# Optimization experiments

Measured on AMD Instinct MI355X. Metric: run time of the kernel, lower is better.

## Reference

```python
import jax, jax.numpy as jnp
import numpy as np

B, S, D = 2, 2048, 2048
G, HPG = 4, 4            # n_groups, heads_per_group (n_heads=16)
DH = D // (G * HPG)      # head dim d_q = d_k = d_v = 128


def setup_inputs() -> dict:
    key = jax.random.key(0)
    ks = jax.random.split(key, 14)
    s = 1.0 / np.sqrt(D)
    inp = {
        "query": jax.random.normal(ks[0], (B, S, D), jnp.float32),
        "key":   jax.random.normal(ks[1], (B, S, D), jnp.float32),
        "value": jax.random.normal(ks[2], (B, S, D), jnp.float32),
        # per-group, per-head Q projections; per-group shared K, V
        "WQ": jax.random.normal(ks[3], (G, HPG, DH, D), jnp.float32) * s,
        "bQ": jax.random.normal(ks[4], (G, HPG, DH), jnp.float32) * 0.01,
        "WK": jax.random.normal(ks[5], (G, DH, D), jnp.float32) * s,
        "bK": jax.random.normal(ks[6], (G, DH), jnp.float32) * 0.01,
        "WV": jax.random.normal(ks[7], (G, DH, D), jnp.float32) * s,
        "bV": jax.random.normal(ks[8], (G, DH), jnp.float32) * 0.01,
        "WO": jax.random.normal(ks[9], (D, G * HPG * DH), jnp.float32) * s,
        "bO": jax.random.normal(ks[10], (D,), jnp.float32) * 0.01,
    }
    return inp


def reference(query, key, value, WQ, bQ, WK, bK, WV, bV, WO, bO):
    # q: [B, G, HPG, S, DH] — all per-head Q projections as one batched GEMM
    q = jnp.einsum('bsd,ghqd->bghsq', query, WQ) + bQ[None, :, :, None, :]
    # k, v: [B, G, S, DH] — one K/V per group (shared across heads in group)
    k = jnp.einsum('bsd,gkd->bgsk', key, WK) + bK[None, :, None, :]
    v = jnp.einsum('bsd,gvd->bgsv', value, WV) + bV[None, :, None, :]
    scale = 1.0 / jnp.sqrt(jnp.asarray(DH, q.dtype))
    # scores: [B, G, HPG, S_q, S_k]
    scores = jnp.einsum('bghsq,bgtq->bghst', q, k) * scale
    attn = jax.nn.softmax(scores, axis=-1)
    out = jnp.einsum('bghst,bgtv->bghsv', attn, v)   # [B, G, HPG, S, DH]
    # concat heads group-major, then transpose(1,2) + flatten like the torch code
    out = out.reshape(B, G * HPG, S, DH).transpose(0, 2, 1, 3).reshape(B, S, G * HPG * DH)
    return out @ WO.T + bO
```

## Files before the change

kernel.cpp:

```cpp
#include <hip/hip_runtime.h>
#include <cstdint>
#include <cstddef>


typedef __attribute__((ext_vector_type(8)))  __bf16 bf16x8;
typedef __attribute__((ext_vector_type(4)))  __bf16 bf16x4;
typedef __attribute__((ext_vector_type(4)))  float  f32x4;
typedef __attribute__((ext_vector_type(16))) float  f32x16;
typedef __attribute__((ext_vector_type(4)))  unsigned int u32x4;

#define GLD16(gp, lp) __builtin_amdgcn_global_load_lds(                         \
    (__attribute__((address_space(1))) void*)(size_t)(gp),                     \
    (__attribute__((address_space(3))) void*)(lp), 16, 0, 0)

#define PLSWAP(a, b) asm volatile("v_permlane32_swap_b32 %0, %1" : "+v"(a), "+v"(b))
#define EXP2F(x) __builtin_amdgcn_exp2f(x)

static __device__ __forceinline__ unsigned pack2bf(float a, float b) {
    unsigned short ua = __builtin_bit_cast(unsigned short, (__bf16)a);
    unsigned short ub = __builtin_bit_cast(unsigned short, (__bf16)b);
    return (unsigned)ua | ((unsigned)ub << 16);
}

__global__ void f2b_kernel(const float* __restrict__ in, __bf16* __restrict__ out, long n8) {
    long stride = (long)gridDim.x * blockDim.x;
    for (long i = (long)blockIdx.x * blockDim.x + threadIdx.x; i < n8; i += stride) {
        const float4* p = (const float4*)(in + i * 8);
        float4 a = p[0], b = p[1];
        bf16x8 r;
        r[0] = (__bf16)a.x; r[1] = (__bf16)a.y; r[2] = (__bf16)a.z; r[3] = (__bf16)a.w;
        r[4] = (__bf16)b.x; r[5] = (__bf16)b.y; r[6] = (__bf16)b.z; r[7] = (__bf16)b.w;
        *(bf16x8*)(out + i * 8) = r;
    }
}

template <int OUTF32>
__global__ __launch_bounds__(512)
void gemm256(const __bf16* __restrict__ A, const __bf16* __restrict__ Bm,
             const float* __restrict__ bias, float* __restrict__ Cf,
             __bf16* __restrict__ Cb, int M, int N, int K, int nbx) {
    __shared__ __bf16 As[3][256 * 64];
    __shared__ __bf16 Bs[3][128 * 64];
    const int tid = threadIdx.x, lane = tid & 63, wid = tid >> 6;
    const int g = lane >> 4, c = lane & 15;
    const int wr = wid >> 1, wc = wid & 1;
    const int cpx = gridDim.x >> 3;
    const int swz = ((int)blockIdx.x & 7) * cpx + ((int)blockIdx.x >> 3);
    const int bx = swz % nbx, by = swz / nbx;
    const int m0 = by * 256, n0 = bx * 128;
    const int nkt = K >> 6;

    const f32x4 z = {0.f, 0.f, 0.f, 0.f};
    f32x4 acc[4][4];
#pragma unroll
    for (int i = 0; i < 4; ++i)
#pragma unroll
        for (int j = 0; j < 4; ++j) acc[i][j] = z;

    auto stageA = [&](int b, int kt, int h) {
        if (kt >= nkt) return;
        const __bf16* src = A + (size_t)m0 * K + (size_t)kt * 64;
#pragma unroll
        for (int i = 0; i < 2; ++i) {
            int ci = h * 1024 + i * 512 + tid;
            int row = ci >> 3, chg = (ci & 7) ^ (row & 7);
            GLD16(src + (size_t)row * K + chg * 8, &As[b][ci * 8]);
        }
    };
    auto stageB = [&](int b, int kt) {
        if (kt >= nkt) return;
        const __bf16* src = Bm + (size_t)n0 * K + (size_t)kt * 64;
#pragma unroll
        for (int i = 0; i < 2; ++i) {
            int ci = i * 512 + tid;
            int row = ci >> 3, chg = (ci & 7) ^ (row & 7);
            GLD16(src + (size_t)row * K + chg * 8, &Bs[b][ci * 8]);
        }
    };

    stageA(0, 0, 0); stageA(0, 0, 1); stageB(0, 0);
    stageA(1, 1, 0); stageA(1, 1, 1); stageB(1, 1);
    asm volatile("s_waitcnt vmcnt(6)" ::: "memory");
    __builtin_amdgcn_sched_barrier(0);
    __builtin_amdgcn_s_barrier();

    int bd = 0;
    for (int kt = 0; kt < nkt; ++kt) {
        const int bs = (bd >= 1) ? bd - 1 : 2;
        bf16x8 af[4], bfr[4];
#pragma unroll
        for (int ph = 0; ph < 2; ++ph) {
#pragma unroll
            for (int mi = 0; mi < 4; ++mi) {
                int row = wr * 64 + mi * 16 + c;
                int ch = (ph * 4 + g) ^ (c & 7);
                af[mi] = *(const bf16x8*)&As[bd][row * 64 + ch * 8];
            }
#pragma unroll
            for (int ni = 0; ni < 4; ++ni) {
                int row = wc * 64 + ni * 16 + c;
                int ch = (ph * 4 + g) ^ (c & 7);
                bfr[ni] = *(const bf16x8*)&Bs[bd][row * 64 + ch * 8];
            }
            if (ph == 0) {
                stageA(bs, kt + 2, 0);
            } else {
                stageA(bs, kt + 2, 1);
                stageB(bs, kt + 2);
            }
            __builtin_amdgcn_s_barrier();
            asm volatile("s_waitcnt lgkmcnt(0)" ::: "memory");
            __builtin_amdgcn_sched_barrier(0);
            __builtin_amdgcn_s_setprio(1);
#pragma unroll
            for (int mi = 0; mi < 4; ++mi)
#pragma unroll
                for (int ni = 0; ni < 4; ++ni)
                    acc[mi][ni] = __builtin_amdgcn_mfma_f32_16x16x32_bf16(
                        af[mi], bfr[ni], acc[mi][ni], 0, 0, 0);
            __builtin_amdgcn_s_setprio(0);
            if (ph == 1) {
                if (kt >= nkt - 2) asm volatile("s_waitcnt vmcnt(0)" ::: "memory");
                else               asm volatile("s_waitcnt vmcnt(6)" ::: "memory");
                __builtin_amdgcn_sched_barrier(0);
            }
            __builtin_amdgcn_s_barrier();
        }
        bd = (bd >= 2) ? 0 : bd + 1;
    }

#pragma unroll
    for (int mi = 0; mi < 4; ++mi) {
#pragma unroll
        for (int ni = 0; ni < 4; ++ni) {
            int col = n0 + wc * 64 + ni * 16 + c;
            float bvc = bias[col];
#pragma unroll
            for (int r = 0; r < 4; ++r) {
                int row = m0 + wr * 64 + mi * 16 + g * 4 + r;
                float v = acc[mi][ni][r] + bvc;
                if (OUTF32) Cf[(size_t)row * N + col] = v;
                else        Cb[(size_t)row * N + col] = (__bf16)v;
            }
        }
    }
}

static __device__ __forceinline__
void gemm_tile(const __bf16* __restrict__ A, const __bf16* __restrict__ Bm,
               const float* __restrict__ bias,
               __bf16* __restrict__ Cb, int N, int K, int m0, int n0, int biasrow,
               __bf16* As, __bf16* Bs) {
    const int tid = threadIdx.x;
    const int lane = tid & 63, wid = tid >> 6;
    const int g = lane >> 4, c = lane & 15;
    const int wr = wid >> 1, wc = wid & 1;

    const f32x4 z = {0.f, 0.f, 0.f, 0.f};
    f32x4 acc[4][4];
#pragma unroll
    for (int i = 0; i < 4; ++i)
#pragma unroll
        for (int j = 0; j < 4; ++j) acc[i][j] = z;

    const int nk = K >> 5;
#pragma unroll
    for (int i = 0; i < 2; ++i) {
        int ci = i * 256 + tid, row = ci >> 2, kc = (ci & 3) * 8;
        GLD16(A + (size_t)(m0 + row) * K + kc, As + ci * 8);
        GLD16(Bm + (size_t)(n0 + row) * K + kc, Bs + ci * 8);
    }
    __syncthreads();

    int cur = 0;
    for (int t = 0; t < nk; ++t) {
        if (t + 1 < nk) {
            int koff = (t + 1) * 32;
            int nb = (cur ^ 1) * 4096;
#pragma unroll
            for (int i = 0; i < 2; ++i) {
                int ci = i * 256 + tid, row = ci >> 2, kc = (ci & 3) * 8;
                GLD16(A + (size_t)(m0 + row) * K + koff + kc, As + nb + ci * 8);
                GLD16(Bm + (size_t)(n0 + row) * K + koff + kc, Bs + nb + ci * 8);
            }
        }
        int cb = cur * 4096;
        bf16x8 af[4], bfv[4];
#pragma unroll
        for (int im = 0; im < 4; ++im)
            af[im] = *(const bf16x8*)&As[cb + (wr * 64 + im * 16 + c) * 32 + g * 8];
#pragma unroll
        for (int in = 0; in < 4; ++in)
            bfv[in] = *(const bf16x8*)&Bs[cb + (wc * 64 + in * 16 + c) * 32 + g * 8];
        __builtin_amdgcn_s_setprio(1);
#pragma unroll
        for (int im = 0; im < 4; ++im)
#pragma unroll
            for (int in = 0; in < 4; ++in)
                acc[im][in] = __builtin_amdgcn_mfma_f32_16x16x32_bf16(
                    af[im], bfv[in], acc[im][in], 0, 0, 0);
        __builtin_amdgcn_s_setprio(0);
        __syncthreads();
        cur ^= 1;
    }

#pragma unroll
    for (int im = 0; im < 4; ++im) {
#pragma unroll
        for (int in = 0; in < 4; ++in) {
            int col = n0 + wc * 64 + in * 16 + c;
            float bvc = biasrow ? 0.f : bias[col];
#pragma unroll
            for (int r = 0; r < 4; ++r) {
                int row = m0 + wr * 64 + im * 16 + g * 4 + r;
                float v = acc[im][in][r] + (biasrow ? bias[row] : bvc);
                Cb[(size_t)row * N + col] = (__bf16)v;
            }
        }
    }
}

__global__ __launch_bounds__(256)
void gemm_kv(const __bf16* __restrict__ kb, const __bf16* __restrict__ wkb,
             const float* __restrict__ bK, __bf16* __restrict__ kp,
             const __bf16* __restrict__ wvb, const __bf16* __restrict__ vb,
             const float* __restrict__ bV, __bf16* __restrict__ vpT) {
    __shared__ __bf16 As[2 * 128 * 32];
    __shared__ __bf16 Bs[2 * 128 * 32];
    const int bid = blockIdx.x;
    const int swz = (bid & 7) * 32 + (bid >> 3);
    if (swz < 128) {
        int bx = swz & 31, by = swz >> 5;
        gemm_tile(kb, wkb, bK, kp, 512, 2048, bx * 128, by * 128, 0, As, Bs);
    } else {
        int s2 = swz - 128;
        int bx = s2 & 3, by = s2 >> 2;
        gemm_tile(wvb, vb, bV, vpT, 4096, 2048, bx * 128, by * 128, 1, As, Bs);
    }
}

__global__ __launch_bounds__(256)
void attn_kernel(const __bf16* __restrict__ Qw, const __bf16* __restrict__ Kw,
                 const __bf16* __restrict__ VTw, __bf16* __restrict__ Ow) {
    constexpr int S = 2048, DQ = 2048, DKV = 512, TOK = 4096;
    const int bid = blockIdx.x;
    const int xcd = bid & 7, slot = bid >> 3;
    const int b = xcd >> 2, grp = xcd & 3;
    const int head = grp * 4 + (slot & 3);
    const int qblk = slot >> 2;
    const __bf16* Q   = Qw + (size_t)b * S * DQ + head * 128;
    const __bf16* Kp  = Kw + (size_t)b * S * DKV + grp * 128;
    const __bf16* VTp = VTw + (size_t)(grp * 128) * TOK + (size_t)b * S;
    __bf16* Op = Ow + (size_t)b * S * DQ + head * 128;

    __shared__ __bf16 Ks[2][64 * 128];
    __shared__ __bf16 Vs[2][128 * 64];

    const int tid = threadIdx.x, wid = tid >> 6, lane = tid & 63;
    const int ql = lane & 31, hi = lane >> 5;
    const int qrow = qblk * 128 + wid * 32 + ql;

    bf16x8 qf[8];
#pragma unroll
    for (int ks = 0; ks < 8; ++ks)
        qf[ks] = *(const bf16x8*)(Q + (size_t)qrow * DQ + ks * 16 + hi * 8);

    f32x16 o[4];
#pragma unroll
    for (int d = 0; d < 4; ++d)
#pragma unroll
        for (int r = 0; r < 16; ++r) o[d][r] = 0.f;
    float mprev = -1e30f, lsum = 0.f;
    constexpr float kexp = 0.08838834764831845f * 1.4426950408889634f;
    constexpr float THR = 8.0f / kexp;

    auto stage = [&](int buf, int t) {
#pragma unroll
        for (int i = 0; i < 4; ++i) {
            int ci = i * 256 + tid;
            int key = ci >> 4, ccl = ci & 15, ccg = ccl ^ (key & 15);
            GLD16(Kp + (size_t)(t * 64 + key) * DKV + ccg * 8, &Ks[buf][ci * 8]);
        }
#pragma unroll
        for (int i = 0; i < 4; ++i) {
            int ci = i * 256 + tid;
            int dh = ci >> 3, cl = ci & 7, cg = cl ^ ((dh ^ (dh >> 3)) & 7);
            GLD16(VTp + (size_t)dh * TOK + t * 64 + cg * 8, &Vs[buf][ci * 8]);
        }
    };

    stage(0, 0);
    __syncthreads();

    const int nt = S / 64;
    int cur = 0;
    for (int t = 0; t < nt; ++t) {
        if (t + 1 < nt) stage(cur ^ 1, t + 1);

        f32x16 sc[2];
        __builtin_amdgcn_s_setprio(1);
#pragma unroll
        for (int kt = 0; kt < 2; ++kt) {
#pragma unroll
            for (int r = 0; r < 16; ++r) sc[kt][r] = 0.f;
#pragma unroll
            for (int ks = 0; ks < 8; ++ks) {
                int key = kt * 32 + ql;
                int chl = (ks * 2 + hi) ^ (key & 15);
                bf16x8 kf = *(const bf16x8*)&Ks[cur][key * 128 + chl * 8];
                sc[kt] = __builtin_amdgcn_mfma_f32_32x32x16_bf16(kf, qf[ks], sc[kt], 0, 0, 0);
            }
        }
        __builtin_amdgcn_s_setprio(0);

        float mo = sc[0][0];
#pragma unroll
        for (int r = 1; r < 16; ++r) mo = fmaxf(mo, sc[0][r]);
#pragma unroll
        for (int r = 0; r < 16; ++r) mo = fmaxf(mo, sc[1][r]);
        mo = fmaxf(mo, __shfl_xor(mo, 32, 64));
        if (!__all(mo - mprev <= THR)) {
            float mn = fmaxf(mprev, mo);
            float ef = EXP2F((mprev - mn) * kexp);
            lsum *= ef;
#pragma unroll
            for (int d = 0; d < 4; ++d)
#pragma unroll
                for (int r = 0; r < 16; ++r) o[d][r] *= ef;
            mprev = mn;
        }
        float mnk = mprev * kexp;
        float rs = 0.f;
#pragma unroll
        for (int kt = 0; kt < 2; ++kt)
#pragma unroll
            for (int r = 0; r < 16; ++r) {
                float p = EXP2F(__builtin_fmaf(sc[kt][r], kexp, -mnk));
                sc[kt][r] = p;
                rs += p;
            }
        rs += __shfl_xor(rs, 32, 64);
        lsum += rs;

        unsigned pk[2][4][2];
#pragma unroll
        for (int kt = 0; kt < 2; ++kt)
#pragma unroll
            for (int rg = 0; rg < 4; ++rg) {
                pk[kt][rg][0] = pack2bf(sc[kt][rg * 4 + 0], sc[kt][rg * 4 + 1]);
                pk[kt][rg][1] = pack2bf(sc[kt][rg * 4 + 2], sc[kt][rg * 4 + 3]);
            }

        __builtin_amdgcn_s_setprio(1);
#pragma unroll
        for (int ks = 0; ks < 4; ++ks) {
            const int kt = ks >> 1, e = ks & 1;
            unsigned a0 = pk[kt][2 * e][0], b0 = pk[kt][2 * e + 1][0];
            unsigned a1 = pk[kt][2 * e][1], b1 = pk[kt][2 * e + 1][1];
            PLSWAP(a0, b0);
            PLSWAP(a1, b1);
            u32x4 fw = {a0, a1, b0, b1};
            bf16x8 pf = __builtin_bit_cast(bf16x8, fw);
#pragma unroll
            for (int dht = 0; dht < 4; ++dht) {
                int dh = dht * 32 + ql;
                int chl = (ks * 2 + hi) ^ ((dh ^ (dh >> 3)) & 7);
                bf16x8 vf = *(const bf16x8*)&Vs[cur][dh * 64 + chl * 8];
                o[dht] = __builtin_amdgcn_mfma_f32_32x32x16_bf16(vf, pf, o[dht], 0, 0, 0);
            }
        }
        __builtin_amdgcn_s_setprio(0);
        __syncthreads();
        cur ^= 1;
    }

    float inv = 1.0f / lsum;
#pragma unroll
    for (int dht = 0; dht < 4; ++dht)
#pragma unroll
        for (int rg = 0; rg < 4; ++rg) {
            bf16x4 wv;
#pragma unroll
            for (int j = 0; j < 4; ++j) wv[j] = (__bf16)(o[dht][rg * 4 + j] * inv);
            int dh0 = dht * 32 + rg * 8 + hi * 4;
            *(bf16x4*)(Op + (size_t)qrow * DQ + dh0) = wv;
        }
}

extern "C" void kernel_launch(void* const* d_in, const int* in_sizes, int n_in,
                              void* d_out, int out_size, void* d_ws, size_t ws_size,
                              hipStream_t stream) {
    (void)in_sizes; (void)n_in; (void)out_size; (void)ws_size;
    const float* query = (const float*)d_in[0];
    const float* key   = (const float*)d_in[1];
    const float* value = (const float*)d_in[2];
    const float* WQ = (const float*)d_in[3];
    const float* bQ = (const float*)d_in[4];
    const float* WK = (const float*)d_in[5];
    const float* bK = (const float*)d_in[6];
    const float* WV = (const float*)d_in[7];
    const float* bV = (const float*)d_in[8];
    const float* WO = (const float*)d_in[9];
    const float* bO = (const float*)d_in[10];
    float* out = (float*)d_out;

    __bf16* w = (__bf16*)d_ws;
    __bf16* qb  = w; w += (size_t)4096 * 2048;
    __bf16* kb  = w; w += (size_t)4096 * 2048;
    __bf16* vb  = w; w += (size_t)4096 * 2048;
    __bf16* wqb = w; w += (size_t)2048 * 2048;
    __bf16* wkb = w; w += (size_t)512 * 2048;
    __bf16* wvb = w; w += (size_t)512 * 2048;
    __bf16* wob = w; w += (size_t)2048 * 2048;
    __bf16* qp  = w; w += (size_t)4096 * 2048;
    __bf16* kp  = w; w += (size_t)4096 * 512;
    __bf16* vpT = w; w += (size_t)512 * 4096;
    __bf16* ao  = w; w += (size_t)4096 * 2048;

    auto conv = [&](const float* src, __bf16* dst, long n) {
        long n8 = n >> 3;
        long blocks = (n8 + 255) / 256;
        if (blocks > 2048) blocks = 2048;
        f2b_kernel<<<(int)blocks, 256, 0, stream>>>(src, dst, n8);
    };
    conv(query, qb, (long)4096 * 2048);
    conv(key,   kb, (long)4096 * 2048);
    conv(value, vb, (long)4096 * 2048);
    conv(WQ, wqb, (long)2048 * 2048);
    conv(WK, wkb, (long)512 * 2048);
    conv(WV, wvb, (long)512 * 2048);
    conv(WO, wob, (long)2048 * 2048);

    gemm256<0><<<256, 512, 0, stream>>>(qb, wqb, bQ, nullptr, qp, 4096, 2048, 2048, 16);
    gemm_kv<<<256, 256, 0, stream>>>(kb, wkb, bK, kp, wvb, vb, bV, vpT);

    attn_kernel<<<512, 256, 0, stream>>>(qp, kp, vpT, ao);

    gemm256<1><<<256, 512, 0, stream>>>(ao, wob, bO, out, nullptr, 4096, 2048, 2048, 16);
}
```

Measured before the change: 292.8 us.

## Software-pipeline QK^T of next tile with PV in attention, merge conversion launches

The attention loop is restructured so that the QK^T MFMAs for tile t+1 are interleaved with the PV MFMAs for tile t. K is triple-buffered and V double-buffered in LDS, and the score registers ping-pong between two sets. Row max and row sum now use tree reductions instead of serial chains. The seven fp32-to-bf16 conversion launches are merged into one multi-segment kernel to cut launch overhead. In exchange the kernel needs more LDS and registers, which may lower occupancy.

```diff
diff --git a/kernel.cpp b/kernel.cpp
--- a/kernel.cpp
+++ b/kernel.cpp
@@ -22,15 +22,25 @@
     return (unsigned)ua | ((unsigned)ub << 16);
 }
 
-__global__ void f2b_kernel(const float* __restrict__ in, __bf16* __restrict__ out, long n8) {
-    long stride = (long)gridDim.x * blockDim.x;
-    for (long i = (long)blockIdx.x * blockDim.x + threadIdx.x; i < n8; i += stride) {
-        const float4* p = (const float4*)(in + i * 8);
-        float4 a = p[0], b = p[1];
+struct F2BArgs {
+    const float* src[7];
+    __bf16* dst[7];
+    long beg[8];
+};
+__global__ void f2b_multi(F2BArgs a) {
+    const long total = a.beg[7];
+    const long stride = (long)gridDim.x * blockDim.x;
+    for (long i = (long)blockIdx.x * blockDim.x + threadIdx.x; i < total; i += stride) {
+        int s = 0;
+#pragma unroll
+        for (int j = 1; j < 7; ++j) s += (i >= a.beg[j]);
+        long off = i - a.beg[s];
+        const float4* p = (const float4*)(a.src[s] + off * 8);
+        float4 x = p[0], y = p[1];
         bf16x8 r;
-        r[0] = (__bf16)a.x; r[1] = (__bf16)a.y; r[2] = (__bf16)a.z; r[3] = (__bf16)a.w;
-        r[4] = (__bf16)b.x; r[5] = (__bf16)b.y; r[6] = (__bf16)b.z; r[7] = (__bf16)b.w;
-        *(bf16x8*)(out + i * 8) = r;
+        r[0] = (__bf16)x.x; r[1] = (__bf16)x.y; r[2] = (__bf16)x.z; r[3] = (__bf16)x.w;
+        r[4] = (__bf16)y.x; r[5] = (__bf16)y.y; r[6] = (__bf16)y.z; r[7] = (__bf16)y.w;
+        *(bf16x8*)(a.dst[s] + off * 8) = r;
     }
 }
 
@@ -243,6 +253,7 @@
 void attn_kernel(const __bf16* __restrict__ Qw, const __bf16* __restrict__ Kw,
                  const __bf16* __restrict__ VTw, __bf16* __restrict__ Ow) {
     constexpr int S = 2048, DQ = 2048, DKV = 512, TOK = 4096;
+    constexpr int nt = S / 64;
     const int bid = blockIdx.x;
     const int xcd = bid & 7, slot = bid >> 3;
     const int b = xcd >> 2, grp = xcd & 3;
@@ -253,7 +264,7 @@
     const __bf16* VTp = VTw + (size_t)(grp * 128) * TOK + (size_t)b * S;
     __bf16* Op = Ow + (size_t)b * S * DQ + head * 128;
 
-    __shared__ __bf16 Ks[2][64 * 128];
+    __shared__ __bf16 Ks[3][64 * 128];
     __shared__ __bf16 Vs[2][128 * 64];
 
     const int tid = threadIdx.x, wid = tid >> 6, lane = tid & 63;
@@ -274,13 +285,15 @@
     constexpr float kexp = 0.08838834764831845f * 1.4426950408889634f;
     constexpr float THR = 8.0f / kexp;
 
-    auto stage = [&](int buf, int t) {
+    auto stageK = [&](int buf, int t) {
 #pragma unroll
         for (int i = 0; i < 4; ++i) {
             int ci = i * 256 + tid;
             int key = ci >> 4, ccl = ci & 15, ccg = ccl ^ (key & 15);
             GLD16(Kp + (size_t)(t * 64 + key) * DKV + ccg * 8, &Ks[buf][ci * 8]);
         }
+    };
+    auto stageV = [&](int buf, int t) {
 #pragma unroll
         for (int i = 0; i < 4; ++i) {
             int ci = i * 256 + tid;
@@ -289,36 +302,39 @@
         }
     };
 
-    stage(0, 0);
+    stageK(0, 0); stageK(1, 1); stageV(0, 0);
     __syncthreads();
 
-    const int nt = S / 64;
-    int cur = 0;
-    for (int t = 0; t < nt; ++t) {
-        if (t + 1 < nt) stage(cur ^ 1, t + 1);
-
-        f32x16 sc[2];
-        __builtin_amdgcn_s_setprio(1);
-#pragma unroll
-        for (int kt = 0; kt < 2; ++kt) {
-#pragma unroll
-            for (int r = 0; r < 16; ++r) sc[kt][r] = 0.f;
-#pragma unroll
-            for (int ks = 0; ks < 8; ++ks) {
-                int key = kt * 32 + ql;
-                int chl = (ks * 2 + hi) ^ (key & 15);
-                bf16x8 kf = *(const bf16x8*)&Ks[cur][key * 128 + chl * 8];
-                sc[kt] = __builtin_amdgcn_mfma_f32_32x32x16_bf16(kf, qf[ks], sc[kt], 0, 0, 0);
-            }
-        }
-        __builtin_amdgcn_s_setprio(0);
-
-        float mo = sc[0][0];
-#pragma unroll
-        for (int r = 1; r < 16; ++r) mo = fmaxf(mo, sc[0][r]);
-#pragma unroll
-        for (int r = 0; r < 16; ++r) mo = fmaxf(mo, sc[1][r]);
-        mo = fmaxf(mo, __shfl_xor(mo, 32, 64));
+    f32x16 scA[2], scB[2];
+#pragma unroll
+    for (int kt = 0; kt < 2; ++kt)
+#pragma unroll
+        for (int r = 0; r < 16; ++r) scA[kt][r] = 0.f;
+    __builtin_amdgcn_s_setprio(1);
+#pragma unroll
+    for (int kt = 0; kt < 2; ++kt)
+#pragma unroll
+        for (int ks = 0; ks < 8; ++ks) {
+            int key = kt * 32 + ql;
+            int chl = (ks * 2 + hi) ^ (key & 15);
+            bf16x8 kf = *(const bf16x8*)&Ks[0][key * 128 + chl * 8];
+            scA[kt] = __builtin_amdgcn_mfma_f32_32x32x16_bf16(kf, qf[ks], scA[kt], 0, 0, 0);
+        }
+    __builtin_amdgcn_s_setprio(0);
+
+    auto body = [&](int t, f32x16 (&scc)[2], f32x16 (&scn)[2]) {
+        const bool hasN = (t + 1) < nt;
+        if (t + 2 < nt) stageK((t + 2) % 3, t + 2);
+        if (hasN)       stageV((t + 1) & 1, t + 1);
+
+        float mx[16];
+#pragma unroll
+        for (int r = 0; r < 16; ++r) mx[r] = fmaxf(scc[0][r], scc[1][r]);
+#pragma unroll
+        for (int w = 8; w >= 1; w >>= 1)
+#pragma unroll
+            for (int r = 0; r < w; ++r) mx[r] = fmaxf(mx[r], mx[r + w]);
+        float mo = fmaxf(mx[0], __shfl_xor(mx[0], 32, 64));
         if (!__all(mo - mprev <= THR)) {
             float mn = fmaxf(mprev, mo);
             float ef = EXP2F((mprev - mn) * kexp);
@@ -330,48 +346,73 @@
             mprev = mn;
         }
         float mnk = mprev * kexp;
-        float rs = 0.f;
 #pragma unroll
         for (int kt = 0; kt < 2; ++kt)
 #pragma unroll
-            for (int r = 0; r < 16; ++r) {
-                float p = EXP2F(__builtin_fmaf(sc[kt][r], kexp, -mnk));
-                sc[kt][r] = p;
-                rs += p;
-            }
-        rs += __shfl_xor(rs, 32, 64);
-        lsum += rs;
+            for (int r = 0; r < 16; ++r)
+                scc[kt][r] = EXP2F(__builtin_fmaf(scc[kt][r], kexp, -mnk));
+        float sm[16];
+#pragma unroll
+        for (int r = 0; r < 16; ++r) sm[r] = scc[0][r] + scc[1][r];
+#pragma unroll
+        for (int w = 8; w >= 1; w >>= 1)
+#pragma unroll
+            for (int r = 0; r < w; ++r) sm[r] += sm[r + w];
+        lsum += sm[0] + __shfl_xor(sm[0], 32, 64);
 
         unsigned pk[2][4][2];
 #pragma unroll
         for (int kt = 0; kt < 2; ++kt)
 #pragma unroll
             for (int rg = 0; rg < 4; ++rg) {
-                pk[kt][rg][0] = pack2bf(sc[kt][rg * 4 + 0], sc[kt][rg * 4 + 1]);
-                pk[kt][rg][1] = pack2bf(sc[kt][rg * 4 + 2], sc[kt][rg * 4 + 3]);
-            }
-
+                pk[kt][rg][0] = pack2bf(scc[kt][rg * 4 + 0], scc[kt][rg * 4 + 1]);
+                pk[kt][rg][1] = pack2bf(scc[kt][rg * 4 + 2], scc[kt][rg * 4 + 3]);
+            }
+
+        const __bf16* kbp = &Ks[(t + 1) % 3][0];
+        const __bf16* vbp = &Vs[t & 1][0];
+        if (hasN) {
+#pragma unroll
+            for (int kt = 0; kt < 2; ++kt)
+#pragma unroll
+                for (int r = 0; r < 16; ++r) scn[kt][r] = 0.f;
+        }
         __builtin_amdgcn_s_setprio(1);
 #pragma unroll
-        for (int ks = 0; ks < 4; ++ks) {
-            const int kt = ks >> 1, e = ks & 1;
-            unsigned a0 = pk[kt][2 * e][0], b0 = pk[kt][2 * e + 1][0];
-            unsigned a1 = pk[kt][2 * e][1], b1 = pk[kt][2 * e + 1][1];
-            PLSWAP(a0, b0);
-            PLSWAP(a1, b1);
-            u32x4 fw = {a0, a1, b0, b1};
-            bf16x8 pf = __builtin_bit_cast(bf16x8, fw);
-#pragma unroll
-            for (int dht = 0; dht < 4; ++dht) {
-                int dh = dht * 32 + ql;
-                int chl = (ks * 2 + hi) ^ ((dh ^ (dh >> 3)) & 7);
-                bf16x8 vf = *(const bf16x8*)&Vs[cur][dh * 64 + chl * 8];
-                o[dht] = __builtin_amdgcn_mfma_f32_32x32x16_bf16(vf, pf, o[dht], 0, 0, 0);
+        for (int ks = 0; ks < 8; ++ks) {
+            if (hasN) {
+#pragma unroll
+                for (int kt = 0; kt < 2; ++kt) {
+                    int key = kt * 32 + ql;
+                    int chl = (ks * 2 + hi) ^ (key & 15);
+                    bf16x8 kf = *(const bf16x8*)&kbp[key * 128 + chl * 8];
+                    scn[kt] = __builtin_amdgcn_mfma_f32_32x32x16_bf16(kf, qf[ks], scn[kt], 0, 0, 0);
+                }
+            }
+            if ((ks & 1) == 0) {
+                const int s = ks >> 1, kt2 = s >> 1, e = s & 1;
+                unsigned a0 = pk[kt2][2 * e][0], b0 = pk[kt2][2 * e + 1][0];
+                unsigned a1 = pk[kt2][2 * e][1], b1 = pk[kt2][2 * e + 1][1];
+                PLSWAP(a0, b0);
+                PLSWAP(a1, b1);
+                u32x4 fw = {a0, a1, b0, b1};
+                bf16x8 pf = __builtin_bit_cast(bf16x8, fw);
+#pragma unroll
+                for (int dht = 0; dht < 4; ++dht) {
+                    int dh = dht * 32 + ql;
+                    int chl = (s * 2 + hi) ^ ((dh ^ (dh >> 3)) & 7);
+                    bf16x8 vf = *(const bf16x8*)&vbp[dh * 64 + chl * 8];
+                    o[dht] = __builtin_amdgcn_mfma_f32_32x32x16_bf16(vf, pf, o[dht], 0, 0, 0);
+                }
             }
         }
         __builtin_amdgcn_s_setprio(0);
         __syncthreads();
-        cur ^= 1;
+    };
+
+    for (int t = 0; t < nt; t += 2) {
+        body(t, scA, scB);
+        body(t + 1, scB, scA);
     }
 
     float inv = 1.0f / lsum;
@@ -417,19 +458,19 @@
     __bf16* vpT = w; w += (size_t)512 * 4096;
     __bf16* ao  = w; w += (size_t)4096 * 2048;
 
-    auto conv = [&](const float* src, __bf16* dst, long n) {
-        long n8 = n >> 3;
-        long blocks = (n8 + 255) / 256;
-        if (blocks > 2048) blocks = 2048;
-        f2b_kernel<<<(int)blocks, 256, 0, stream>>>(src, dst, n8);
-    };
-    conv(query, qb, (long)4096 * 2048);
-    conv(key,   kb, (long)4096 * 2048);
-    conv(value, vb, (long)4096 * 2048);
-    conv(WQ, wqb, (long)2048 * 2048);
-    conv(WK, wkb, (long)512 * 2048);
-    conv(WV, wvb, (long)512 * 2048);
-    conv(WO, wob, (long)2048 * 2048);
+    F2BArgs fa;
+    fa.src[0] = query; fa.dst[0] = qb;
+    fa.src[1] = key;   fa.dst[1] = kb;
+    fa.src[2] = value; fa.dst[2] = vb;
+    fa.src[3] = WQ;    fa.dst[3] = wqb;
+    fa.src[4] = WK;    fa.dst[4] = wkb;
+    fa.src[5] = WV;    fa.dst[5] = wvb;
+    fa.src[6] = WO;    fa.dst[6] = wob;
+    const long n8s[7] = {1048576, 1048576, 1048576, 524288, 131072, 131072, 524288};
+    long acc = 0;
+    for (int i = 0; i < 7; ++i) { fa.beg[i] = acc; acc += n8s[i]; }
+    fa.beg[7] = acc;
+    f2b_multi<<<2048, 256, 0, stream>>>(fa);
 
     gemm256<0><<<256, 512, 0, stream>>>(qb, wqb, bQ, nullptr, qp, 4096, 2048, 2048, 16);
     gemm_kv<<<256, 256, 0, stream>>>(kb, wkb, bK, kp, wvb, vb, bV, vpT);
```

After: 292.3 us. About the same (-0.2%).
